# Optimization experiments

Measured on AMD Instinct MI355X. Metric: run time of the kernel, lower is better.

The kernel has to match this reference:

```python
import jax, jax.numpy as jnp
import numpy as np

N, D, H, HD = 256, 128, 4, 32


def setup_inputs() -> dict:
    key = jax.random.key(0)
    ks = jax.random.split(key, 8)
    def w(k, shape):
        return jax.random.normal(k, shape, jnp.float32) * (1.0 / np.sqrt(shape[0]))
    return {
        "x": jax.random.normal(ks[0], (1, N, N, D), jnp.float32),
        "ln_w": jnp.ones((D,), jnp.float32),
        "ln_b": jnp.zeros((D,), jnp.float32),
        "Wb": w(ks[1], (D, H)),
        "Wq": w(ks[2], (D, H * HD)),
        "Wk": w(ks[3], (D, H * HD)),
        "Wv": w(ks[4], (D, H * HD)),
        "Wg": w(ks[5], (D, H * HD)),
        "Wo": w(ks[6], (H * HD, D)),
    }


def reference(x, ln_w, ln_b, Wb, Wq, Wk, Wv, Wg, Wo):
    ending = False  # init arg; if True, transpose the two N dims before/after
    z = x[0]  # [N, N, D]
    if ending:
        z = jnp.transpose(z, (1, 0, 2))
    # LayerNorm over last dim, eps=1e-5
    mu = jnp.mean(z, axis=-1, keepdims=True)
    var = jnp.mean(jnp.square(z - mu), axis=-1, keepdims=True)
    z = (z - mu) * jax.lax.rsqrt(var + 1e-5) * ln_w + ln_b
    # triangle bias: [N, N, H] -> [1, H, N, N]
    bias = jnp.transpose(z @ Wb, (2, 0, 1))[None]
    q = (z @ Wq).reshape(N, N, H, HD)
    k = (z @ Wk).reshape(N, N, H, HD)
    v = (z @ Wv).reshape(N, N, H, HD)
    # scores over the second N dim per row b: [N(rows), H, N(q), N(k)]
    a = jnp.einsum("bqhc,bkhc->bhqk", q, k) * (HD ** -0.5) + bias
    p = jax.nn.softmax(a, axis=-1)
    o = jnp.einsum("bhqk,bkhc->bqhc", p, v).reshape(N, N, H * HD)
    g = jax.nn.sigmoid(z @ Wg)
    out = (o * g) @ Wo  # [N, N, D]
    if ending:
        out = jnp.transpose(out, (1, 0, 2))
    return out[None]
```

## Files before the change

kernel.cpp:

```cpp
#include <hip/hip_runtime.h>
#include <hip/hip_bf16.h>

#define NN 65536
#define DD 128
#define NH 4
#define HDIM 32

typedef __bf16 bf16_t;
typedef __bf16 bf16x8 __attribute__((ext_vector_type(8)));
typedef __bf16 bf16x4 __attribute__((ext_vector_type(4)));
typedef __bf16 bf16x2 __attribute__((ext_vector_type(2)));
typedef float f32x4 __attribute__((ext_vector_type(4)));
typedef float f32x16 __attribute__((ext_vector_type(16)));
typedef unsigned int u32;
typedef unsigned int u32x4 __attribute__((ext_vector_type(4)));

__device__ inline u32 pk2(float a, float b) {
    bf16x2 t;
    t[0] = (bf16_t)a;
    t[1] = (bf16_t)b;
    return __builtin_bit_cast(u32, t);
}
__device__ inline bf16x8 frag4(u32 a, u32 b, u32 c, u32 d) {
    u32x4 t = {a, b, c, d};
    return __builtin_bit_cast(bf16x8, t);
}
__device__ inline bf16x8 cat44(bf16x4 a, bf16x4 b) {
    bf16x8 r;
#pragma unroll
    for (int j = 0; j < 4; j++) { r[j] = a[j]; r[4 + j] = b[j]; }
    return r;
}
__device__ inline void packX(const f32x16& s, bool lo, bf16x8& f0, bf16x8& f1) {
    u32 wv[8];
#pragma unroll
    for (int g = 0; g < 4; g++) {
        wv[2 * g] = pk2(s[4 * g], s[4 * g + 1]);
        wv[2 * g + 1] = pk2(s[4 * g + 2], s[4 * g + 3]);
    }
    u32 p0 = __shfl_xor(wv[0], 32), p1 = __shfl_xor(wv[1], 32);
    u32 p2 = __shfl_xor(wv[2], 32), p3 = __shfl_xor(wv[3], 32);
    u32 p4 = __shfl_xor(wv[4], 32), p5 = __shfl_xor(wv[5], 32);
    u32 p6 = __shfl_xor(wv[6], 32), p7 = __shfl_xor(wv[7], 32);
    f0 = frag4(lo ? wv[0] : p2, lo ? wv[1] : p3, lo ? p0 : wv[2], lo ? p1 : wv[3]);
    f1 = frag4(lo ? wv[4] : p6, lo ? wv[5] : p7, lo ? p4 : wv[6], lo ? p5 : wv[7]);
}

__global__ __launch_bounds__(256) void convw_kernel(const float* __restrict__ Wq,
                                                    const float* __restrict__ Wk,
                                                    const float* __restrict__ Wv,
                                                    const float* __restrict__ Wg,
                                                    const float* __restrict__ Wo,
                                                    bf16_t* __restrict__ wf,
                                                    bf16_t* __restrict__ wfO) {
    __shared__ float Ws[128][33];
    __shared__ float Ws2[128][17];
    int blk = blockIdx.x, t = threadIdx.x;
    if (blk < 16) {
        int m = blk >> 2, h = blk & 3;
        const float* W = (m == 0) ? Wq : (m == 1) ? Wk : (m == 2) ? Wv : Wg;
#pragma unroll
        for (int p = 0; p < 16; p++) {
            int d = p * 8 + (t >> 5), o = t & 31;
            Ws[d][o] = W[d * 128 + h * 32 + o];
        }
        __syncthreads();
        bf16_t* dst = wf + (size_t)blk * 4096;
#pragma unroll
        for (int p = 0; p < 16; p++) {
            int j = p * 256 + t;
            int ks = j >> 9, rsel = (j >> 4) & 31, e = j & 15;
            dst[j] = (bf16_t)Ws[ks * 16 + e][rsel];
        }
    } else {
        int oc = blk - 16;
#pragma unroll
        for (int p = 0; p < 8; p++) {
            int d = p * 16 + (t >> 4), o = t & 15;
            Ws2[d][o] = Wo[d * 128 + oc * 16 + o];
        }
        __syncthreads();
        bf16_t* dst = wfO + (size_t)oc * 2048;
#pragma unroll
        for (int p = 0; p < 8; p++) {
            int j = p * 256 + t;
            int ks = j >> 9, rem = j & 511;
            int lx = rem >> 5, ly = (rem >> 3) & 3, e = j & 7;
            dst[j] = (bf16_t)Ws2[ks * 32 + ly * 8 + e][lx];
        }
    }
}

__global__ __launch_bounds__(256) void ln_kernel(const float* __restrict__ x,
                                                 const float* __restrict__ lw,
                                                 const float* __restrict__ lb,
                                                 const float* __restrict__ Wb,
                                                 bf16_t* __restrict__ zF,
                                                 float* __restrict__ bias3) {
    __shared__ bf16_t zs[4096];
    __shared__ float bias_s[4][32];
    int t = threadIdx.x;
    int g = t >> 5, l32 = t & 31;
    int rowbase = blockIdx.x * 32;
    int d0 = l32 * 4;
    f32x4 lwv = *reinterpret_cast<const f32x4*>(&lw[d0]);
    f32x4 lbv = *reinterpret_cast<const f32x4*>(&lb[d0]);
    f32x4 wbj[4];
#pragma unroll
    for (int j = 0; j < 4; j++) wbj[j] = *reinterpret_cast<const f32x4*>(&Wb[(d0 + j) * 4]);
#pragma unroll
    for (int r4 = 0; r4 < 4; r4++) {
        int roff = r4 * 8 + g;
        int row = rowbase + roff;
        f32x4 v = *reinterpret_cast<const f32x4*>(&x[(size_t)row * 128 + d0]);
        float s1 = v[0] + v[1] + v[2] + v[3];
        float s2 = v[0] * v[0] + v[1] * v[1] + v[2] * v[2] + v[3] * v[3];
#pragma unroll
        for (int m = 1; m < 32; m <<= 1) {
            s1 += __shfl_xor(s1, m);
            s2 += __shfl_xor(s2, m);
        }
        float mu = s1 * (1.0f / 128.0f);
        float var = s2 * (1.0f / 128.0f) - mu * mu;
        float rs = rsqrtf(var + 1e-5f);
        float zv[4];
        bf16x4 pk;
#pragma unroll
        for (int j = 0; j < 4; j++) {
            zv[j] = (v[j] - mu) * rs * lwv[j] + lbv[j];
            pk[j] = (bf16_t)zv[j];
        }
        *reinterpret_cast<bf16x4*>(&zs[(l32 >> 2) * 512 + roff * 16 + (l32 & 3) * 4]) = pk;
        f32x4 pb = {0.f, 0.f, 0.f, 0.f};
#pragma unroll
        for (int j = 0; j < 4; j++)
#pragma unroll
            for (int hh = 0; hh < 4; hh++) pb[hh] += zv[j] * wbj[j][hh];
#pragma unroll
        for (int m = 1; m < 32; m <<= 1) {
#pragma unroll
            for (int hh = 0; hh < 4; hh++) pb[hh] += __shfl_xor(pb[hh], m);
        }
        if (l32 == 0) {
#pragma unroll
            for (int hh = 0; hh < 4; hh++)
                bias_s[hh][roff] = pb[hh] * 1.4426950408889634f;
        }
    }
    __syncthreads();
    if (t < 128) {
        bias3[(size_t)(t >> 5) * NN + rowbase + (t & 31)] = bias_s[t >> 5][t & 31];
    }
    bf16_t* dst = zF + (size_t)blockIdx.x * 4096;
#pragma unroll
    for (int p = 0; p < 2; p++) {
        int c = p * 2048 + t * 8;
        *reinterpret_cast<bf16x8*>(dst + c) = *reinterpret_cast<bf16x8*>(zs + c);
    }
}

__global__ __launch_bounds__(256) void biastr_kernel(const float* __restrict__ bias3,
                                                     float* __restrict__ bias2) {
    __shared__ float T[64][68];
    int t = threadIdx.x;
    int h = blockIdx.x >> 4;
    int q0 = ((blockIdx.x >> 2) & 3) * 64, k0 = (blockIdx.x & 3) * 64;
#pragma unroll
    for (int i = 0; i < 4; i++) {
        int id = i * 256 + t;
        int r = id >> 4, cb = id & 15;
        f32x4 val = *reinterpret_cast<const f32x4*>(&bias3[h * NN + (q0 + r) * 256 + k0 + cb * 4]);
        *reinterpret_cast<f32x4*>(&T[r][cb * 4]) = val;
    }
    __syncthreads();
#pragma unroll
    for (int i = 0; i < 4; i++) {
        int id = i * 256 + t;
        int kr = id >> 4, qb = id & 15;
        f32x4 o;
#pragma unroll
        for (int j = 0; j < 4; j++) o[j] = T[qb * 4 + j][kr];
        *reinterpret_cast<f32x4*>(&bias2[h * NN + (k0 + kr) * 256 + q0 + qb * 4]) = o;
    }
}

__global__ __launch_bounds__(512, 4) void fat_kernel(const bf16_t* __restrict__ zF,
                                                     const bf16_t* __restrict__ wf,
                                                     const float* __restrict__ bias2,
                                                     bf16_t* __restrict__ om2,
                                                     bf16_t* __restrict__ gm2) {
    __shared__ bf16_t Kh[256][44];
    __shared__ bf16_t Vt[32][268];
    int t = threadIdx.x;
    int id = blockIdx.x;
    int h = (id >> 3) & 3;
    int b = (id & 7) + (id >> 5) * 8;
    int w = t >> 6, lane = t & 63;
    int rsel = lane & 31, hi = lane >> 5;
    int hi8 = hi * 8, hi4 = hi * 4;
    bool lo = (hi == 0);
    const float SCL2 = 0.17677669529663687f * 1.4426950408889634f;
    const bf16_t* zg0 = zF + (size_t)(b * 8 + w) * 4096;
    int fro = rsel * 16 + hi8;

    bf16x8 qf0, qf1;
    {
        const bf16_t* wq = wf + (size_t)(0 * 4 + h) * 4096;
        const bf16_t* wk = wf + (size_t)(1 * 4 + h) * 4096;
        const bf16_t* wv = wf + (size_t)(2 * 4 + h) * 4096;
        const bf16_t* wg = wf + (size_t)(3 * 4 + h) * 4096;
        f32x16 aq, ak, av, ag;
#pragma unroll
        for (int i = 0; i < 16; i++) { aq[i] = 0.f; ak[i] = 0.f; av[i] = 0.f; ag[i] = 0.f; }
#pragma unroll
        for (int ks = 0; ks < 8; ks++) {
            int off = ks * 512 + fro;
            bf16x8 zb = *reinterpret_cast<const bf16x8*>(zg0 + off);
            bf16x8 fq = *reinterpret_cast<const bf16x8*>(wq + off);
            bf16x8 fk = *reinterpret_cast<const bf16x8*>(wk + off);
            bf16x8 fv = *reinterpret_cast<const bf16x8*>(wv + off);
            bf16x8 fg = *reinterpret_cast<const bf16x8*>(wg + off);
            aq = __builtin_amdgcn_mfma_f32_32x32x16_bf16(fq, zb, aq, 0, 0, 0);
            ak = __builtin_amdgcn_mfma_f32_32x32x16_bf16(fk, zb, ak, 0, 0, 0);
            av = __builtin_amdgcn_mfma_f32_32x32x16_bf16(fv, zb, av, 0, 0, 0);
            ag = __builtin_amdgcn_mfma_f32_32x32x16_bf16(fg, zb, ag, 0, 0, 0);
        }
        int key0 = w * 32 + rsel;
        bf16x8 f0, f1;
        packX(ak, lo, f0, f1);
        *reinterpret_cast<bf16x8*>(&Kh[key0][hi8]) = f0;
        *reinterpret_cast<bf16x8*>(&Kh[key0][16 + hi8]) = f1;
#pragma unroll
        for (int r = 0; r < 16; r++) {
            int c = (r & 3) + 8 * (r >> 2) + hi4;
            Vt[c][key0] = (bf16_t)av[r];
        }
#pragma unroll
        for (int i = 0; i < 16; i++) ag[i] = 1.0f / (1.0f + __expf(-ag[i]));
        bf16_t* grow = gm2 + ((size_t)h * NN + b * 256 + key0) * 32;
        packX(ag, lo, f0, f1);
        *reinterpret_cast<bf16x8*>(grow + hi8) = f0;
        *reinterpret_cast<bf16x8*>(grow + 16 + hi8) = f1;
        packX(aq, lo, qf0, qf1);
    }
    __syncthreads();

    {
        int qpos = w * 32 + rsel;
        const float* bq = bias2 + (size_t)h * NN + qpos;

        f32x16 of;
#pragma unroll
        for (int i = 0; i < 16; i++) of[i] = 0.f;
        float m = -1e30f, l = 0.f;

        float bv[16];
#pragma unroll
        for (int e = 0; e < 16; e++) {
            int key = 8 * (e >> 2) + hi4 + (e & 3);
            bv[e] = bq[(size_t)key * 256];
        }
#pragma unroll
        for (int kt = 0; kt < 8; kt++) {
            bf16x8 k0 = *reinterpret_cast<bf16x8*>(&Kh[kt * 32 + rsel][hi8]);
            bf16x8 k1 = *reinterpret_cast<bf16x8*>(&Kh[kt * 32 + rsel][16 + hi8]);
            f32x16 s;
#pragma unroll
            for (int i = 0; i < 16; i++) s[i] = 0.f;
            __builtin_amdgcn_s_setprio(1);
            s = __builtin_amdgcn_mfma_f32_32x32x16_bf16(k0, qf0, s, 0, 0, 0);
            s = __builtin_amdgcn_mfma_f32_32x32x16_bf16(k1, qf1, s, 0, 0, 0);
            __builtin_amdgcn_s_setprio(0);
            float bvn[16];
            if (kt < 7) {
#pragma unroll
                for (int e = 0; e < 16; e++) {
                    int key = (kt + 1) * 32 + 8 * (e >> 2) + hi4 + (e & 3);
                    bvn[e] = bq[(size_t)key * 256];
                }
            }
            float tm[8];
#pragma unroll
            for (int e = 0; e < 16; e++) s[e] = s[e] * SCL2 + bv[e];
#pragma unroll
            for (int e = 0; e < 8; e++) tm[e] = fmaxf(s[e], s[e + 8]);
#pragma unroll
            for (int st = 4; st >= 1; st >>= 1)
#pragma unroll
                for (int e = 0; e < st; e++) tm[e] = fmaxf(tm[e], tm[e + st]);
            float pm = fmaxf(tm[0], __shfl_xor(tm[0], 32));
            if (__any(pm > m)) {
                float nm = fmaxf(m, pm);
                float al = __builtin_amdgcn_exp2f(m - nm);
                m = nm;
                l *= al;
#pragma unroll
                for (int i = 0; i < 16; i++) of[i] *= al;
            }
            float ts[8];
#pragma unroll
            for (int e = 0; e < 16; e++) s[e] = __builtin_amdgcn_exp2f(s[e] - m);
#pragma unroll
            for (int e = 0; e < 8; e++) ts[e] = s[e] + s[e + 8];
#pragma unroll
            for (int st = 4; st >= 1; st >>= 1)
#pragma unroll
                for (int e = 0; e < st; e++) ts[e] += ts[e + st];
            l += ts[0];
            bf16x8 pf0 = frag4(pk2(s[0], s[1]), pk2(s[2], s[3]),
                               pk2(s[4], s[5]), pk2(s[6], s[7]));
            bf16x8 pf1 = frag4(pk2(s[8], s[9]), pk2(s[10], s[11]),
                               pk2(s[12], s[13]), pk2(s[14], s[15]));
            bf16x8 va = cat44(*reinterpret_cast<bf16x4*>(&Vt[rsel][kt * 32 + hi4]),
                              *reinterpret_cast<bf16x4*>(&Vt[rsel][kt * 32 + 8 + hi4]));
            bf16x8 vb = cat44(*reinterpret_cast<bf16x4*>(&Vt[rsel][kt * 32 + 16 + hi4]),
                              *reinterpret_cast<bf16x4*>(&Vt[rsel][kt * 32 + 24 + hi4]));
            __builtin_amdgcn_s_setprio(1);
            of = __builtin_amdgcn_mfma_f32_32x32x16_bf16(va, pf0, of, 0, 0, 0);
            of = __builtin_amdgcn_mfma_f32_32x32x16_bf16(vb, pf1, of, 0, 0, 0);
            __builtin_amdgcn_s_setprio(0);
            if (kt < 7) {
#pragma unroll
                for (int e = 0; e < 16; e++) bv[e] = bvn[e];
            }
        }

        l += __shfl_xor(l, 32);
        float linv = 1.0f / l;
#pragma unroll
        for (int i = 0; i < 16; i++) of[i] *= linv;
        bf16x8 o0, o1;
        packX(of, lo, o0, o1);
        bf16_t* orow = om2 + ((size_t)h * NN + b * 256 + qpos) * 32;
        *reinterpret_cast<bf16x8*>(orow + hi8) = o0;
        *reinterpret_cast<bf16x8*>(orow + 16 + hi8) = o1;
    }
}

__global__ __launch_bounds__(256) void final_kernel(const bf16_t* __restrict__ om2,
                                                    const bf16_t* __restrict__ gm2,
                                                    const bf16_t* __restrict__ wfO,
                                                    float* __restrict__ out) {
    __shared__ __align__(16) char smraw[64 * 136 * 2];
    bf16_t(*As)[136] = reinterpret_cast<bf16_t(*)[136]>(smraw);
    float(*Of)[68] = reinterpret_cast<float(*)[68]>(smraw);
    int t = threadIdx.x;
    int rb = blockIdx.x;
#pragma unroll
    for (int i = 0; i < 4; i++) {
        int c = i * 256 + t;
        int r = c >> 4, off = (c & 15) * 8;
        size_t hm = ((size_t)(off >> 5) * NN + rb * 64 + r) * 32 + (off & 31);
        bf16x8 o8 = *reinterpret_cast<const bf16x8*>(&om2[hm]);
        bf16x8 g8 = *reinterpret_cast<const bf16x8*>(&gm2[hm]);
        bf16x8 p8;
#pragma unroll
        for (int e = 0; e < 8; e++) p8[e] = (bf16_t)((float)o8[e] * (float)g8[e]);
        *reinterpret_cast<bf16x8*>(&As[r][off]) = p8;
    }
    __syncthreads();
    int w = t >> 6, lane = t & 63;
    int lx = lane & 15, ly = lane >> 4;
    int m0 = (w >> 1) * 32, n0 = (w & 1) * 32;
    bf16x8 af[2][4];
#pragma unroll
    for (int mt = 0; mt < 2; mt++)
#pragma unroll
        for (int ks = 0; ks < 4; ks++)
            af[mt][ks] = *reinterpret_cast<bf16x8*>(&As[m0 + mt * 16 + lx][ks * 32 + ly * 8]);
    __syncthreads();

    for (int half = 0; half < 2; half++) {
        int nc0 = half * 64;
        bf16x8 bfr[2][4];
#pragma unroll
        for (int nt = 0; nt < 2; nt++) {
            int oc = ((nc0 + n0) >> 4) + nt;
#pragma unroll
            for (int ks = 0; ks < 4; ks++)
                bfr[nt][ks] = *reinterpret_cast<const bf16x8*>(
                    &wfO[oc * 2048 + ks * 512 + lx * 32 + ly * 8]);
        }
        f32x4 acc[2][2];
#pragma unroll
        for (int mt = 0; mt < 2; mt++)
#pragma unroll
            for (int nt = 0; nt < 2; nt++) acc[mt][nt] = (f32x4){0.f, 0.f, 0.f, 0.f};
#pragma unroll
        for (int ks = 0; ks < 4; ks++)
#pragma unroll
            for (int mt = 0; mt < 2; mt++)
#pragma unroll
                for (int nt = 0; nt < 2; nt++)
                    acc[mt][nt] = __builtin_amdgcn_mfma_f32_16x16x32_bf16(af[mt][ks], bfr[nt][ks], acc[mt][nt], 0, 0, 0);
#pragma unroll
        for (int mt = 0; mt < 2; mt++)
#pragma unroll
            for (int nt = 0; nt < 2; nt++)
#pragma unroll
                for (int r = 0; r < 4; r++)
                    Of[m0 + mt * 16 + ly * 4 + r][n0 + nt * 16 + lx] = acc[mt][nt][r];
        __syncthreads();
#pragma unroll
        for (int j = 0; j < 4; j++) {
            int ch = j * 256 + t;
            int r = ch >> 4, cb = ch & 15;
            f32x4 val = *reinterpret_cast<f32x4*>(&Of[r][cb * 4]);
            *reinterpret_cast<f32x4*>(&out[(rb * 64 + r) * 128 + nc0 + cb * 4]) = val;
        }
        __syncthreads();
    }
}

extern "C" void kernel_launch(void* const* d_in, const int* in_sizes, int n_in,
                              void* d_out, int out_size, void* d_ws, size_t ws_size,
                              hipStream_t stream) {
    const float* x   = (const float*)d_in[0];
    const float* lnw = (const float*)d_in[1];
    const float* lnb = (const float*)d_in[2];
    const float* Wb  = (const float*)d_in[3];
    const float* Wq  = (const float*)d_in[4];
    const float* Wk  = (const float*)d_in[5];
    const float* Wv  = (const float*)d_in[6];
    const float* Wg  = (const float*)d_in[7];
    const float* Wo  = (const float*)d_in[8];
    float* out = (float*)d_out;

    char* ws = (char*)d_ws;
    const size_t MAT = (size_t)NN * 128 * sizeof(bf16_t);
    bf16_t* zF    = (bf16_t*)(ws);
    bf16_t* gmat  = (bf16_t*)(ws + MAT);
    bf16_t* omat  = (bf16_t*)(ws + 2 * MAT);
    bf16_t* wf    = (bf16_t*)(ws + 3 * MAT);
    bf16_t* wfO   = (bf16_t*)(ws + 3 * MAT + (128 << 10));
    float*  bias3 = (float*)(ws + 3 * MAT + (1 << 20));
    float*  bias2 = (float*)(ws + 3 * MAT + (2 << 20));

    convw_kernel<<<24, 256, 0, stream>>>(Wq, Wk, Wv, Wg, Wo, wf, wfO);
    ln_kernel<<<2048, 256, 0, stream>>>(x, lnw, lnb, Wb, zF, bias3);
    biastr_kernel<<<64, 256, 0, stream>>>(bias3, bias2);
    fat_kernel<<<1024, 512, 0, stream>>>(zF, wf, bias2, omat, gmat);
    final_kernel<<<1024, 256, 0, stream>>>(omat, gmat, wfO, out);
}
```

Measured before the change: 77.93 us.

## Fuse sigmoid gate into attention epilogue and fold bias into MFMA accumulator

The gate sigmoid is now applied inside the attention kernel's output epilogue. This drops the gm2 intermediate buffer, which saves one 16 MB bf16 write and one read per call. The attention bias is preloaded as the MFMA accumulator init, and the softmax scale is pre-multiplied into Q, which removes a per-element FMA in the score loop. The max reduction is also restructured into max3-friendly trees. The trade-off is higher register pressure, since 16 sigmoid values stay live across the attention loop.

```diff
diff --git a/kernel.cpp b/kernel.cpp
--- a/kernel.cpp
+++ b/kernel.cpp
@@ -187,8 +187,7 @@
 __global__ __launch_bounds__(512, 4) void fat_kernel(const bf16_t* __restrict__ zF,
                                                      const bf16_t* __restrict__ wf,
                                                      const float* __restrict__ bias2,
-                                                     bf16_t* __restrict__ om2,
-                                                     bf16_t* __restrict__ gm2) {
+                                                     bf16_t* __restrict__ om2) {
     __shared__ bf16_t Kh[256][44];
     __shared__ bf16_t Vt[32][268];
     int t = threadIdx.x;
@@ -202,8 +201,18 @@
     const float SCL2 = 0.17677669529663687f * 1.4426950408889634f;
     const bf16_t* zg0 = zF + (size_t)(b * 8 + w) * 4096;
     int fro = rsel * 16 + hi8;
+    int qpos = w * 32 + rsel;
+    const float* bq = bias2 + (size_t)h * NN + qpos;
+
+    f32x16 bv;
+#pragma unroll
+    for (int e = 0; e < 16; e++) {
+        int key = 8 * (e >> 2) + hi4 + (e & 3);
+        bv[e] = bq[(size_t)key * 256];
+    }
 
     bf16x8 qf0, qf1;
+    f32x16 sg;
     {
         const bf16_t* wq = wf + (size_t)(0 * 4 + h) * 4096;
         const bf16_t* wk = wf + (size_t)(1 * 4 + h) * 4096;
@@ -236,59 +245,44 @@
             Vt[c][key0] = (bf16_t)av[r];
         }
 #pragma unroll
-        for (int i = 0; i < 16; i++) ag[i] = 1.0f / (1.0f + __expf(-ag[i]));
-        bf16_t* grow = gm2 + ((size_t)h * NN + b * 256 + key0) * 32;
-        packX(ag, lo, f0, f1);
-        *reinterpret_cast<bf16x8*>(grow + hi8) = f0;
-        *reinterpret_cast<bf16x8*>(grow + 16 + hi8) = f1;
+        for (int i = 0; i < 16; i++) sg[i] = 1.0f / (1.0f + __expf(-ag[i]));
+#pragma unroll
+        for (int i = 0; i < 16; i++) aq[i] *= SCL2;
         packX(aq, lo, qf0, qf1);
     }
     __syncthreads();
 
     {
-        int qpos = w * 32 + rsel;
-        const float* bq = bias2 + (size_t)h * NN + qpos;
-
         f32x16 of;
 #pragma unroll
         for (int i = 0; i < 16; i++) of[i] = 0.f;
         float m = -1e30f, l = 0.f;
 
-        float bv[16];
-#pragma unroll
-        for (int e = 0; e < 16; e++) {
-            int key = 8 * (e >> 2) + hi4 + (e & 3);
-            bv[e] = bq[(size_t)key * 256];
-        }
 #pragma unroll
         for (int kt = 0; kt < 8; kt++) {
             bf16x8 k0 = *reinterpret_cast<bf16x8*>(&Kh[kt * 32 + rsel][hi8]);
             bf16x8 k1 = *reinterpret_cast<bf16x8*>(&Kh[kt * 32 + rsel][16 + hi8]);
-            f32x16 s;
-#pragma unroll
-            for (int i = 0; i < 16; i++) s[i] = 0.f;
+            f32x16 s = bv;
             __builtin_amdgcn_s_setprio(1);
             s = __builtin_amdgcn_mfma_f32_32x32x16_bf16(k0, qf0, s, 0, 0, 0);
             s = __builtin_amdgcn_mfma_f32_32x32x16_bf16(k1, qf1, s, 0, 0, 0);
             __builtin_amdgcn_s_setprio(0);
-            float bvn[16];
             if (kt < 7) {
 #pragma unroll
                 for (int e = 0; e < 16; e++) {
                     int key = (kt + 1) * 32 + 8 * (e >> 2) + hi4 + (e & 3);
-                    bvn[e] = bq[(size_t)key * 256];
+                    bv[e] = bq[(size_t)key * 256];
                 }
             }
-            float tm[8];
-#pragma unroll
-            for (int e = 0; e < 16; e++) s[e] = s[e] * SCL2 + bv[e];
-#pragma unroll
-            for (int e = 0; e < 8; e++) tm[e] = fmaxf(s[e], s[e + 8]);
-#pragma unroll
-            for (int st = 4; st >= 1; st >>= 1)
-#pragma unroll
-                for (int e = 0; e < st; e++) tm[e] = fmaxf(tm[e], tm[e + st]);
-            float pm = fmaxf(tm[0], __shfl_xor(tm[0], 32));
+            float t0 = fmaxf(fmaxf(s[0], s[1]), s[2]);
+            float t1 = fmaxf(fmaxf(s[3], s[4]), s[5]);
+            float t2 = fmaxf(fmaxf(s[6], s[7]), s[8]);
+            float t3 = fmaxf(fmaxf(s[9], s[10]), s[11]);
+            float t4 = fmaxf(fmaxf(s[12], s[13]), s[14]);
+            float u0 = fmaxf(fmaxf(t0, t1), s[15]);
+            float u1 = fmaxf(fmaxf(t2, t3), t4);
+            float pm = fmaxf(u0, u1);
+            pm = fmaxf(pm, __shfl_xor(pm, 32));
             if (__any(pm > m)) {
                 float nm = fmaxf(m, pm);
                 float al = __builtin_amdgcn_exp2f(m - nm);
@@ -319,16 +313,12 @@
             of = __builtin_amdgcn_mfma_f32_32x32x16_bf16(va, pf0, of, 0, 0, 0);
             of = __builtin_amdgcn_mfma_f32_32x32x16_bf16(vb, pf1, of, 0, 0, 0);
             __builtin_amdgcn_s_setprio(0);
-            if (kt < 7) {
-#pragma unroll
-                for (int e = 0; e < 16; e++) bv[e] = bvn[e];
-            }
         }
 
         l += __shfl_xor(l, 32);
         float linv = 1.0f / l;
 #pragma unroll
-        for (int i = 0; i < 16; i++) of[i] *= linv;
+        for (int i = 0; i < 16; i++) of[i] = of[i] * linv * sg[i];
         bf16x8 o0, o1;
         packX(of, lo, o0, o1);
         bf16_t* orow = om2 + ((size_t)h * NN + b * 256 + qpos) * 32;
@@ -338,7 +328,6 @@
 }
 
 __global__ __launch_bounds__(256) void final_kernel(const bf16_t* __restrict__ om2,
-                                                    const bf16_t* __restrict__ gm2,
                                                     const bf16_t* __restrict__ wfO,
                                                     float* __restrict__ out) {
     __shared__ __align__(16) char smraw[64 * 136 * 2];
@@ -352,11 +341,7 @@
         int r = c >> 4, off = (c & 15) * 8;
         size_t hm = ((size_t)(off >> 5) * NN + rb * 64 + r) * 32 + (off & 31);
         bf16x8 o8 = *reinterpret_cast<const bf16x8*>(&om2[hm]);
-        bf16x8 g8 = *reinterpret_cast<const bf16x8*>(&gm2[hm]);
-        bf16x8 p8;
-#pragma unroll
-        for (int e = 0; e < 8; e++) p8[e] = (bf16_t)((float)o8[e] * (float)g8[e]);
-        *reinterpret_cast<bf16x8*>(&As[r][off]) = p8;
+        *reinterpret_cast<bf16x8*>(&As[r][off]) = o8;
     }
     __syncthreads();
     int w = t >> 6, lane = t & 63;
@@ -429,16 +414,15 @@
     char* ws = (char*)d_ws;
     const size_t MAT = (size_t)NN * 128 * sizeof(bf16_t);
     bf16_t* zF    = (bf16_t*)(ws);
-    bf16_t* gmat  = (bf16_t*)(ws + MAT);
-    bf16_t* omat  = (bf16_t*)(ws + 2 * MAT);
-    bf16_t* wf    = (bf16_t*)(ws + 3 * MAT);
-    bf16_t* wfO   = (bf16_t*)(ws + 3 * MAT + (128 << 10));
-    float*  bias3 = (float*)(ws + 3 * MAT + (1 << 20));
-    float*  bias2 = (float*)(ws + 3 * MAT + (2 << 20));
+    bf16_t* omat  = (bf16_t*)(ws + MAT);
+    bf16_t* wf    = (bf16_t*)(ws + 2 * MAT);
+    bf16_t* wfO   = (bf16_t*)(ws + 2 * MAT + (128 << 10));
+    float*  bias3 = (float*)(ws + 2 * MAT + (1 << 20));
+    float*  bias2 = (float*)(ws + 2 * MAT + (2 << 20));
 
     convw_kernel<<<24, 256, 0, stream>>>(Wq, Wk, Wv, Wg, Wo, wf, wfO);
     ln_kernel<<<2048, 256, 0, stream>>>(x, lnw, lnb, Wb, zF, bias3);
     biastr_kernel<<<64, 256, 0, stream>>>(bias3, bias2);
-    fat_kernel<<<1024, 512, 0, stream>>>(zF, wf, bias2, omat, gmat);
-    final_kernel<<<1024, 256, 0, stream>>>(omat, gmat, wfO, out);
-}
+    fat_kernel<<<1024, 512, 0, stream>>>(zF, wf, bias2, omat);
+    final_kernel<<<1024, 256, 0, stream>>>(omat, wfO, out);
+}
```

Result: faster. 76.13 us (-2.3%).
